# Performance work log

Measured on AMD Instinct MI355X. Metric: run time of the kernel, lower is better.

## Reference

```python
import jax, jax.numpy as jnp
import numpy as np

B, H = 1, 512
NVAR, NCLS = 16384, 65536
NP, NM = 4096, 4096
NEG = -1e30


def setup_inputs() -> dict:
    key = jax.random.key(0)
    ks = jax.random.split(key, 16)
    s = 0.02  # weight init scale
    return {
        "literal_emb": jax.random.normal(ks[0], (B, 2 * NVAR, H), jnp.float32),
        "clause_emb": jax.random.normal(ks[1], (B, NCLS, H), jnp.float32),
        "pos_idx": jax.random.randint(ks[2], (NP,), 0, NCLS),
        "neg_idx": jax.random.randint(ks[3], (NM,), 0, NCLS),
        "keep_mask": jax.random.randint(ks[4], (NP, NM), 0, 2).astype(bool),
        "taken_mask": jax.random.uniform(ks[5], (NP, NM)) < 0.01,  # sparse exclusion set
        "var_K_w": s * jax.random.normal(ks[6], (H, H), jnp.float32),
        "var_K_b": jnp.zeros((H,), jnp.float32),
        "var_Q_w": s * jax.random.normal(ks[7], (H, H), jnp.float32),
        "var_Q_b": jnp.zeros((H,), jnp.float32),
        "var_attn_w": s * jax.random.normal(ks[8], (1, H), jnp.float32),
        "var_attn_b": jnp.zeros((1,), jnp.float32),
        "W_Q_w": s * jax.random.normal(ks[9], (H, H), jnp.float32),
        "W_Q_b": jnp.zeros((H,), jnp.float32),
        "W_K_w": s * jax.random.normal(ks[10], (H, H), jnp.float32),
        "W_K_b": jnp.zeros((H,), jnp.float32),
    }


def reference(literal_emb, clause_emb, pos_idx, neg_idx, keep_mask, taken_mask,
              var_K_w, var_K_b, var_Q_w, var_Q_b, var_attn_w, var_attn_b,
              W_Q_w, W_Q_b, W_K_w, W_K_b):
    n_vars = literal_emb.shape[1] // 2
    # --- select_var: additive attention over positive literals ---
    K = literal_emb[:, :n_vars]                       # [B, V, H]
    K_t = K @ var_K_w.T + var_K_b                     # [B, V, H]
    Q = clause_emb.sum(axis=1)                        # [B, H] (C_aggr='sum')
    Q_t = Q @ var_Q_w.T + var_Q_b                     # [B, H]
    u = (jnp.tanh(K_t + Q_t[:, None, :]) @ var_attn_w.T + var_attn_b)[..., 0]  # [B, V]
    log_score = jax.nn.log_softmax(u, axis=-1)
    var_logp = jnp.max(log_score, axis=-1)            # [B]
    var_idx = jnp.argmax(log_score, axis=-1)          # [B]
    # --- clause-pair attention over pivot pos/neg clause pools ---
    q = clause_emb[:, pos_idx] @ W_Q_w.T + W_Q_b      # [B, NP, H]
    k = clause_emb[:, neg_idx] @ W_K_w.T + W_K_b      # [B, NM, H]
    h = q.shape[-1]
    scores = jnp.einsum('bnh,bmh->bnm', q, k) / jnp.sqrt(jnp.float32(h))
    # mask_grid_asym: drop invalid (keep_mask==0) and already-taken pairs, log-normalize
    valid = keep_mask & (~taken_mask)                 # [NP, NM]
    masked = jnp.where(valid[None], scores, jnp.float32(NEG))
    flat = masked.reshape(masked.shape[0], -1)        # [B, NP*NM]
    logp = jax.nn.log_softmax(flat, axis=-1)
    C_logp = jnp.max(logp, axis=-1)                   # [B]
    C_flat = jnp.argmax(logp, axis=-1)                # [B]
    M = scores.shape[-1]
    ci, cj = C_flat // M, C_flat % M
    c_idx_pos = pos_idx[ci]                           # map back to global clause ids
    c_idx_neg = neg_idx[cj]
    c_logp = C_logp + var_logp                        # [B]
    return (c_logp, c_idx_pos, c_idx_neg, var_idx)
```

## Files before the change

### kernel.cpp

```cpp
#include <hip/hip_runtime.h>
#include <hip/hip_bf16.h>
#include <math.h>

#define HH 512
#define NVARS 16384
#define NPOS 4096
#define NMS 4096
#define NEGV -1.0e30f
#define RSQRT_H 0.04419417382415922f

typedef unsigned short u16;
typedef __attribute__((ext_vector_type(8))) short bf16x8;
typedef __attribute__((ext_vector_type(4))) float f32x4;

struct SPart { float m; float s; int a; int pad; };

__device__ inline u16 f2bf(float f) {
  unsigned u = __float_as_uint(f);
  unsigned r = (u + 0x7fffu + ((u >> 16) & 1u)) >> 16;
  return (u16)r;
}
__device__ inline float bf2f(u16 h) { return __uint_as_float(((unsigned)h) << 16); }

__device__ inline void wreduce_maxidx(float& v, int& idx) {
#pragma unroll
  for (int m = 1; m < 64; m <<= 1) {
    float ov = __shfl_xor(v, m, 64);
    int oi = __shfl_xor(idx, m, 64);
    if (ov > v || (ov == v && oi < idx)) { v = ov; idx = oi; }
  }
}

__device__ inline float wreduce_sum(float v) {
#pragma unroll
  for (int m = 1; m < 64; m <<= 1) v += __shfl_xor(v, m, 64);
  return v;
}

__device__ __forceinline__ void stage_frag(const u16* src, u16* dst) {
  __builtin_amdgcn_global_load_lds(
      (const __attribute__((address_space(1))) void*)src,
      (__attribute__((address_space(3))) void*)dst, 16, 0, 0);
}

__device__ __forceinline__ void do_tofrag(
    const float* __restrict__ src, u16* __restrict__ hi, u16* __restrict__ lo,
    int frag, int lane) {
  const int R = frag >> 4, K = frag & 15;
  const float* p = src + (size_t)(R * 16 + (lane & 15)) * HH + K * 32 + (lane >> 4) * 8;
  float v[8];
  *(float4*)&v[0] = *(const float4*)p;
  *(float4*)&v[4] = *(const float4*)(p + 4);
  u16 h[8], l[8];
#pragma unroll
  for (int e = 0; e < 8; ++e) { h[e] = f2bf(v[e]); l[e] = f2bf(v[e] - bf2f(h[e])); }
  size_t base = (size_t)frag * 512 + (size_t)lane * 8;
  *(ushort4*)(hi + base) = *(ushort4*)&h[0];
  *(ushort4*)(hi + base + 4) = *(ushort4*)&h[4];
  *(ushort4*)(lo + base) = *(ushort4*)&l[0];
  *(ushort4*)(lo + base + 4) = *(ushort4*)&l[4];
}

__global__ __launch_bounds__(256) void prep_kernel(
    const void* __restrict__ keep, const void* __restrict__ taken,
    unsigned long long* __restrict__ vmask,
    const float* __restrict__ clause, double* __restrict__ qpart,
    const float* __restrict__ lit, u16* __restrict__ lithi, u16* __restrict__ litlo,
    const float* __restrict__ varKw, u16* __restrict__ wkhi, u16* __restrict__ wklo,
    const float* __restrict__ WQw, u16* __restrict__ pwqhi, u16* __restrict__ pwqlo,
    const float* __restrict__ WKw, u16* __restrict__ pwkhi, u16* __restrict__ pwklo) {
  const int bid = blockIdx.x;
  const int t = threadIdx.x;
  if (bid < 1024) {
    const int fg = t & 127;
    const int rh = t >> 7;
    const float* base = clause + (size_t)(bid * 64 + rh * 32) * HH + fg * 4;
    double a0 = 0.0, a1 = 0.0, a2 = 0.0, a3 = 0.0;
    for (int r0 = 0; r0 < 32; r0 += 8) {
      float4 v[8];
#pragma unroll
      for (int u = 0; u < 8; ++u)
        v[u] = *(const float4*)(base + (size_t)(r0 + u) * HH);
#pragma unroll
      for (int u = 0; u < 8; ++u) {
        a0 += (double)v[u].x; a1 += (double)v[u].y;
        a2 += (double)v[u].z; a3 += (double)v[u].w;
      }
    }
    double* o = qpart + (size_t)(bid * 2 + rh) * HH + fg * 4;
    o[0] = a0; o[1] = a1; o[2] = a2; o[3] = a3;
  } else if (bid < 5120) {
    const int frag = (bid - 1024) * 4 + (t >> 6);
    do_tofrag(lit, lithi, litlo, frag, t & 63);
  } else if (bid < 9216) {
    __shared__ unsigned short us[256];
    const int row = bid - 5120;
    const unsigned* kw = (const unsigned*)keep;
    int f = 1;
#pragma unroll
    for (int i = 0; i < 16; ++i) f &= (kw[i] <= 1u);
    const size_t e = (size_t)row * 4096 + (size_t)t * 16;
    unsigned b = 0;
    if (f) {
      const unsigned* kp = (const unsigned*)keep + e;
      const unsigned* tp = (const unsigned*)taken + e;
#pragma unroll
      for (int c = 0; c < 4; ++c) {
        uint4 kv = *(const uint4*)(kp + c * 4);
        uint4 tv = *(const uint4*)(tp + c * 4);
        b |= (unsigned)(kv.x && !tv.x) << (c * 4 + 0);
        b |= (unsigned)(kv.y && !tv.y) << (c * 4 + 1);
        b |= (unsigned)(kv.z && !tv.z) << (c * 4 + 2);
        b |= (unsigned)(kv.w && !tv.w) << (c * 4 + 3);
      }
    } else {
      uint4 kv = *(const uint4*)((const unsigned char*)keep + e);
      uint4 tv = *(const uint4*)((const unsigned char*)taken + e);
      unsigned kws[4] = {kv.x, kv.y, kv.z, kv.w};
      unsigned tws[4] = {tv.x, tv.y, tv.z, tv.w};
#pragma unroll
      for (int c = 0; c < 4; ++c)
#pragma unroll
        for (int y = 0; y < 4; ++y) {
          unsigned kb = (kws[c] >> (8 * y)) & 0xffu;
          unsigned tb = (tws[c] >> (8 * y)) & 0xffu;
          b |= (unsigned)(kb && !tb) << (c * 4 + y);
        }
    }
    us[t] = (unsigned short)b;
    __syncthreads();
    if (t < 64) {
      unsigned long long m =
          (unsigned long long)us[t * 4 + 0] |
          ((unsigned long long)us[t * 4 + 1] << 16) |
          ((unsigned long long)us[t * 4 + 2] << 32) |
          ((unsigned long long)us[t * 4 + 3] << 48);
      vmask[(size_t)row * 64 + t] = m;
    }
  } else {
    const int wb = bid - 9216;
    const int m = wb >> 7;
    const int frag = (wb & 127) * 4 + (t >> 6);
    const float* src = (m == 0) ? varKw : (m == 1) ? WQw : WKw;
    u16* hi = (m == 0) ? wkhi : (m == 1) ? pwqhi : pwkhi;
    u16* lo = (m == 0) ? wklo : (m == 1) ? pwqlo : pwklo;
    do_tofrag(src, hi, lo, frag, t & 63);
  }
}

__global__ __launch_bounds__(256) void qred_kernel(
    const double* __restrict__ qpart, double* __restrict__ Qd) {
  __shared__ double red[256];
  const int t = threadIdx.x;
  const int h = blockIdx.x * 16 + (t & 15);
  const int chunk = t >> 4;
  double s = 0.0;
  for (int j0 = 0; j0 < 128; j0 += 8) {
    double v[8];
#pragma unroll
    for (int u = 0; u < 8; ++u)
      v[u] = qpart[(size_t)(chunk * 128 + j0 + u) * HH + h];
#pragma unroll
    for (int u = 0; u < 8; ++u) s += v[u];
  }
  red[t] = s;
  __syncthreads();
  for (int off = 8; off > 0; off >>= 1) {
    if (chunk < off) red[t] += red[t + off * 16];
    __syncthreads();
  }
  if (t < 16) Qd[blockIdx.x * 16 + t] = red[t];
}

__global__ __launch_bounds__(256) void prepmv_kernel(
    const double* __restrict__ Qd, const float* __restrict__ varQw,
    const float* __restrict__ varQb, const float* __restrict__ varKb,
    float* __restrict__ tvec) {
  __shared__ double red[256];
  const int t = threadIdx.x;
  const int h = blockIdx.x * 16 + (t & 15);
  const int chunk = t >> 4;
  const float* wrow = varQw + (size_t)h * HH + chunk * 32;
  const double* qd = Qd + chunk * 32;
  double s = 0.0;
  for (int j = 0; j < 32; ++j) s += qd[j] * (double)wrow[j];
  red[t] = s;
  __syncthreads();
  for (int off = 8; off > 0; off >>= 1) {
    if (chunk < off) red[t] += red[t + off * 16];
    __syncthreads();
  }
  if (t < 16) {
    int hh = blockIdx.x * 16 + t;
    tvec[hh] = (float)(red[t] + (double)varQb[hh] + (double)varKb[hh]);
  }
}

#define MFMA16(A, B)                                                                 \
  _Pragma("unroll") for (int i_ = 0; i_ < 4; ++i_)                                   \
  _Pragma("unroll") for (int j_ = 0; j_ < 4; ++j_)                                   \
    acc[i_][j_] = __builtin_amdgcn_mfma_f32_16x16x32_bf16(A[i_], B[j_], acc[i_][j_], 0, 0, 0);

#define MFMAS(AH, AL, BH, BL)                                                        \
  do { MFMA16(AH, BH) MFMA16(AH, BL) MFMA16(AL, BH) } while (0)

__global__ __launch_bounds__(256, 3) void proj_kernel(
    const float* __restrict__ clause,
    const int* __restrict__ pos_idx, const int* __restrict__ neg_idx,
    const u16* __restrict__ pwqhi, const u16* __restrict__ pwqlo,
    const u16* __restrict__ pwkhi, const u16* __restrict__ pwklo,
    const float* __restrict__ bQ, const float* __restrict__ bK,
    u16* __restrict__ qhi, u16* __restrict__ qlo,
    u16* __restrict__ khi, u16* __restrict__ klo) {
  const int* __restrict__ idx = blockIdx.z ? neg_idx : pos_idx;
  const u16* __restrict__ whp = blockIdx.z ? pwkhi : pwqhi;
  const u16* __restrict__ wlp = blockIdx.z ? pwklo : pwqlo;
  const float* __restrict__ bias = blockIdx.z ? bK : bQ;
  u16* __restrict__ ohi = blockIdx.z ? khi : qhi;
  u16* __restrict__ olo = blockIdx.z ? klo : qlo;

  const int t = threadIdx.x, lane = t & 63, wid = t >> 6;
  const int wn = wid & 1, wm = wid >> 1;
  const int row0 = blockIdx.x * 128;
  const int col0 = blockIdx.y * 128;

  const float* bptr[4];
#pragma unroll
  for (int j = 0; j < 4; ++j) {
    int g = idx[row0 + wn * 64 + j * 16 + (lane & 15)];
    bptr[j] = clause + (size_t)g * HH + (lane >> 4) * 8;
  }
  const size_t abase = (size_t)((col0 >> 4) + wm * 4) * 8192 + (size_t)lane * 8;

  f32x4 acc[4][4] = {};
#pragma unroll
  for (int s = 0; s < 16; ++s) {
    float rB[4][8];
    bf16x8 aH[4], aL[4], bH[4], bL[4];
#pragma unroll
    for (int f = 0; f < 4; ++f) {
      *(float4*)&rB[f][0] = *(const float4*)(bptr[f] + s * 32);
      *(float4*)&rB[f][4] = *(const float4*)(bptr[f] + s * 32 + 4);
      size_t oa = abase + (size_t)f * 8192 + (size_t)s * 512;
      aH[f] = *(const bf16x8*)(whp + oa);
      aL[f] = *(const bf16x8*)(wlp + oa);
    }
#pragma unroll
    for (int f = 0; f < 4; ++f)
#pragma unroll
      for (int e = 0; e < 8; ++e) {
        float v = rB[f][e];
        u16 h = f2bf(v);
        bH[f][e] = (short)h;
        bL[f][e] = (short)f2bf(v - bf2f(h));
      }
    MFMA16(aH, bH)
    MFMA16(aL, bH)
    MFMA16(aH, bL)
  }

  const int q4 = lane >> 4;
#pragma unroll
  for (int i = 0; i < 4; ++i) {
    const int hbase = col0 + wm * 64 + i * 16 + q4 * 4;
    float b0 = bias[hbase + 0], b1 = bias[hbase + 1];
    float b2 = bias[hbase + 2], b3 = bias[hbase + 3];
    const int lane16 = (lane & 15) + ((i & 1) * 2 + (q4 >> 1)) * 16;
    const int sub = (q4 & 1) * 4;
#pragma unroll
    for (int j = 0; j < 4; ++j) {
      const int frag = ((row0 + wn * 64 + j * 16) >> 4) * 16 +
                       ((col0 + wm * 64 + i * 16) >> 5);
      size_t base = (size_t)frag * 512 + (size_t)lane16 * 8 + sub;
      ushort4 hv, lv;
      float v;
      v = acc[i][j][0] + b0; hv.x = f2bf(v); lv.x = f2bf(v - bf2f(hv.x));
      v = acc[i][j][1] + b1; hv.y = f2bf(v); lv.y = f2bf(v - bf2f(hv.y));
      v = acc[i][j][2] + b2; hv.z = f2bf(v); lv.z = f2bf(v - bf2f(hv.z));
      v = acc[i][j][3] + b3; hv.w = f2bf(v); lv.w = f2bf(v - bf2f(hv.w));
      *(ushort4*)(ohi + base) = hv;
      *(ushort4*)(olo + base) = lv;
    }
  }
}

__global__ __launch_bounds__(256, 2) void ktu_kernel(
    const u16* __restrict__ lithi, const u16* __restrict__ litlo,
    const u16* __restrict__ wkhi, const u16* __restrict__ wklo,
    const float* __restrict__ tvec, const float* __restrict__ attnw,
    float* __restrict__ upart) {
  __shared__ __align__(16) u16 lds[2][4][8][512];
  const int t = threadIdx.x, lane = t & 63, wid = t >> 6;
  const int wn = wid & 1, wm = wid >> 1;
  const int row0 = blockIdx.x * 128;
  const int l8 = lane * 8;

  const u16* sa = (wid == 0) ? lithi : (wid == 1) ? litlo : (wid == 2) ? wkhi : wklo;
  const int rb = (wid < 2) ? (row0 >> 4) : (blockIdx.y * 8);
  const u16* sab = sa + (size_t)rb * 8192 + l8;

#define KSTAGE(buf, s)                                                        \
  _Pragma("unroll") for (int f_ = 0; f_ < 8; ++f_)                            \
    stage_frag(sab + (size_t)f_ * 8192 + (size_t)(s) * 512,                   \
               &lds[buf][wid][f_][0]);

  KSTAGE(0, 0)
  f32x4 acc[4][4] = {};
#pragma unroll
  for (int s = 0; s < 16; ++s) {
    __syncthreads();
    if (s < 15) { KSTAGE((s + 1) & 1, s + 1) }
    const int b = s & 1;
    bf16x8 aH[4], aL[4], bH[4], bL[4];
#pragma unroll
    for (int f = 0; f < 4; ++f) {
      aH[f] = *(const bf16x8*)&lds[b][0][wn * 4 + f][l8];
      aL[f] = *(const bf16x8*)&lds[b][1][wn * 4 + f][l8];
      bH[f] = *(const bf16x8*)&lds[b][2][wm * 4 + f][l8];
      bL[f] = *(const bf16x8*)&lds[b][3][wm * 4 + f][l8];
    }
    MFMAS(aH, aL, bH, bL);
  }
#undef KSTAGE

  const int cbase = blockIdx.y * 128 + wm * 64;
  float tv[4], aw[4];
#pragma unroll
  for (int j = 0; j < 4; ++j) {
    int c = cbase + j * 16 + (lane & 15);
    tv[j] = tvec[c]; aw[j] = attnw[c];
  }
  float us[4][4];
#pragma unroll
  for (int i = 0; i < 4; ++i)
#pragma unroll
    for (int r = 0; r < 4; ++r) {
      float s = 0.f;
#pragma unroll
      for (int j = 0; j < 4; ++j) {
        float x = acc[i][j][r] + tv[j];
        float th = 1.0f - 2.0f / (__expf(2.0f * x) + 1.0f);
        s += th * aw[j];
      }
      us[i][r] = s;
    }
#pragma unroll
  for (int m = 1; m < 16; m <<= 1)
#pragma unroll
    for (int i = 0; i < 4; ++i)
#pragma unroll
      for (int r = 0; r < 4; ++r) us[i][r] += __shfl_xor(us[i][r], m, 64);
  if ((lane & 15) == 0) {
#pragma unroll
    for (int i = 0; i < 4; ++i)
#pragma unroll
      for (int r = 0; r < 4; ++r) {
        int row = row0 + wn * 64 + i * 16 + (lane >> 4) * 4 + r;
        upart[(size_t)(blockIdx.y * 2 + wm) * NVARS + row] = us[i][r];
      }
  }
}

__global__ __launch_bounds__(256, 2) void scores_kernel(
    const u16* __restrict__ qhi, const u16* __restrict__ qlo,
    const u16* __restrict__ khi, const u16* __restrict__ klo,
    const unsigned long long* __restrict__ vmask, SPart* __restrict__ parts) {
  __shared__ __align__(16) u16 lds[2][4][8][512];
  __shared__ unsigned long long mrow[128][2];
  __shared__ float s_rv[4]; __shared__ int s_ri[4]; __shared__ float s_rs[4];
  __shared__ float s_bm; __shared__ int s_ba;

  const int t = threadIdx.x;
  const int lane = t & 63;
  const int wid = t >> 6;
  const int wn = wid & 1, wm = wid >> 1;
  const int l8 = lane * 8;

  const int bid = blockIdx.x;
  const int xcd = bid & 7, p = bid >> 3;
  const int sp = p >> 6, q = p & 63;
  const int g = xcd * 2 + sp;
  const int bx = (g & 3) * 8 + (q & 7);
  const int by = (g >> 2) * 8 + (q >> 3);

  const int n0 = by * 128;
  const int m0 = bx * 128;

  const u16* sa = (wid == 0) ? qhi : (wid == 1) ? qlo : (wid == 2) ? khi : klo;
  const int rb = (wid < 2) ? (n0 >> 4) : (m0 >> 4);
  const u16* sab = sa + (size_t)rb * 8192 + l8;

#define SSTAGE(buf, s)                                                        \
  _Pragma("unroll") for (int f_ = 0; f_ < 8; ++f_)                            \
    stage_frag(sab + (size_t)f_ * 8192 + (size_t)(s) * 512,                   \
               &lds[buf][wid][f_][0]);

  {
    int r = t >> 1, w = t & 1;
    mrow[r][w] = vmask[(size_t)(n0 + r) * (NMS / 64) + (m0 >> 6) + w];
  }

  SSTAGE(0, 0)
  f32x4 acc[4][4] = {};
#pragma unroll
  for (int s = 0; s < 16; ++s) {
    __syncthreads();
    if (s < 15) { SSTAGE((s + 1) & 1, s + 1) }
    const int b = s & 1;
    bf16x8 aH[4], aL[4], bH[4], bL[4];
#pragma unroll
    for (int f = 0; f < 4; ++f) {
      aH[f] = *(const bf16x8*)&lds[b][0][wn * 4 + f][l8];
      aL[f] = *(const bf16x8*)&lds[b][1][wn * 4 + f][l8];
      bH[f] = *(const bf16x8*)&lds[b][2][wm * 4 + f][l8];
      bL[f] = *(const bf16x8*)&lds[b][3][wm * 4 + f][l8];
    }
    MFMAS(aH, aL, bH, bL);
  }
#undef SSTAGE

  const int rbase = wn * 64 + (lane >> 4) * 4;
  const int cb15 = (lane & 15);

  float mv = NEGV; int mi = 0x7fffffff;
#pragma unroll
  for (int i = 0; i < 4; ++i) {
#pragma unroll
    for (int r = 0; r < 4; ++r) {
      int rl = rbase + i * 16 + r;
      unsigned long long ww = mrow[rl][wm];
      int gb = (n0 + rl) * NMS + m0;
#pragma unroll
      for (int j = 0; j < 4; ++j) {
        int bit = j * 16 + cb15;
        int cl = wm * 64 + bit;
        float sv = acc[i][j][r] * RSQRT_H;
        acc[i][j][r] = sv;
        bool valid = ((ww >> bit) & 1ull) != 0;
        if (valid && (sv > mv || (sv == mv && gb + cl < mi))) { mv = sv; mi = gb + cl; }
      }
    }
  }
  wreduce_maxidx(mv, mi);
  if ((t & 63) == 0) { s_rv[wid] = mv; s_ri[wid] = mi; }
  __syncthreads();
  if (t == 0) {
    float bm = s_rv[0]; int ba = s_ri[0];
    for (int w = 1; w < 4; ++w)
      if (s_rv[w] > bm || (s_rv[w] == bm && s_ri[w] < ba)) { bm = s_rv[w]; ba = s_ri[w]; }
    s_bm = bm; s_ba = ba;
  }
  __syncthreads();
  const float bm = s_bm;

  float se = 0.f;
#pragma unroll
  for (int i = 0; i < 4; ++i) {
#pragma unroll
    for (int r = 0; r < 4; ++r) {
      int rl = rbase + i * 16 + r;
      unsigned long long ww = mrow[rl][wm];
#pragma unroll
      for (int j = 0; j < 4; ++j) {
        int bit = j * 16 + cb15;
        bool valid = ((ww >> bit) & 1ull) != 0;
        if (valid) se += __expf(acc[i][j][r] - bm);
      }
    }
  }
  se = wreduce_sum(se);
  if ((t & 63) == 0) s_rs[wid] = se;
  __syncthreads();
  if (t == 0) {
    SPart pt;
    pt.m = s_bm;
    pt.s = s_rs[0] + s_rs[1] + s_rs[2] + s_rs[3];
    pt.a = s_ba; pt.pad = 0;
    parts[by * 32 + bx] = pt;
  }
}

__global__ __launch_bounds__(256) void usum_kernel(
    const float* __restrict__ upart, SPart* __restrict__ uparts2) {
  __shared__ float s_rv[4]; __shared__ int s_ri[4]; __shared__ float s_rs[4];
  __shared__ float s_bm; __shared__ int s_ba;
  const int t = threadIdx.x;
  const int i = blockIdx.x * 256 + t;
  float u = 0.f;
#pragma unroll
  for (int p = 0; p < 8; ++p) u += upart[(size_t)p * NVARS + i];
  float mv = u; int mi = i;
  wreduce_maxidx(mv, mi);
  if ((t & 63) == 0) { s_rv[t >> 6] = mv; s_ri[t >> 6] = mi; }
  __syncthreads();
  if (t == 0) {
    float bm = s_rv[0]; int ba = s_ri[0];
    for (int w = 1; w < 4; ++w)
      if (s_rv[w] > bm || (s_rv[w] == bm && s_ri[w] < ba)) { bm = s_rv[w]; ba = s_ri[w]; }
    s_bm = bm; s_ba = ba;
  }
  __syncthreads();
  float se = __expf(u - s_bm);
  se = wreduce_sum(se);
  if ((t & 63) == 0) s_rs[t >> 6] = se;
  __syncthreads();
  if (t == 0) {
    SPart p;
    p.m = s_bm;
    p.s = s_rs[0] + s_rs[1] + s_rs[2] + s_rs[3];
    p.a = s_ba; p.pad = 0;
    uparts2[blockIdx.x] = p;
  }
}

__global__ __launch_bounds__(256) void final_kernel(
    const SPart* __restrict__ uparts2, const SPart* __restrict__ parts,
    const int* __restrict__ pos_idx, const int* __restrict__ neg_idx,
    float* __restrict__ out) {
  __shared__ float s_rv[4]; __shared__ int s_ri[4]; __shared__ float s_rs[4];
  __shared__ float s_umax; __shared__ int s_uarg; __shared__ float s_usum;
  __shared__ float s_gm; __shared__ int s_ga;
  const int t = threadIdx.x;

  float mv = -3.0e38f; int mi = 0x7fffffff;
  SPart up;
  if (t < 64) {
    up = uparts2[t];
    mv = up.m; mi = up.a;
  }
  wreduce_maxidx(mv, mi);
  if ((t & 63) == 0) { s_rv[t >> 6] = mv; s_ri[t >> 6] = mi; }
  __syncthreads();
  if (t == 0) {
    float bm = s_rv[0]; int ba = s_ri[0];
    for (int w = 1; w < 4; ++w)
      if (s_rv[w] > bm || (s_rv[w] == bm && s_ri[w] < ba)) { bm = s_rv[w]; ba = s_ri[w]; }
    s_umax = bm; s_uarg = ba;
  }
  __syncthreads();
  float se = (t < 64) ? up.s * __expf(up.m - s_umax) : 0.f;
  se = wreduce_sum(se);
  if ((t & 63) == 0) s_rs[t >> 6] = se;
  __syncthreads();
  if (t == 0) s_usum = s_rs[0] + s_rs[1] + s_rs[2] + s_rs[3];
  __syncthreads();

  mv = NEGV; mi = 0x7fffffff;
  for (int i = t; i < 1024; i += 256) {
    SPart p = parts[i];
    if (p.m > mv || (p.m == mv && p.a < mi)) { mv = p.m; mi = p.a; }
  }
  wreduce_maxidx(mv, mi);
  if ((t & 63) == 0) { s_rv[t >> 6] = mv; s_ri[t >> 6] = mi; }
  __syncthreads();
  if (t == 0) {
    float bm = s_rv[0]; int ba = s_ri[0];
    for (int w = 1; w < 4; ++w)
      if (s_rv[w] > bm || (s_rv[w] == bm && s_ri[w] < ba)) { bm = s_rv[w]; ba = s_ri[w]; }
    s_gm = bm; s_ga = ba;
  }
  __syncthreads();
  const float gm = s_gm;
  float ss = 0.f;
  for (int i = t; i < 1024; i += 256) {
    SPart p = parts[i];
    ss += p.s * __expf(p.m - gm);
  }
  ss = wreduce_sum(ss);
  if ((t & 63) == 0) s_rs[t >> 6] = ss;
  __syncthreads();
  if (t == 0) {
    float gsum = s_rs[0] + s_rs[1] + s_rs[2] + s_rs[3];
    float c_logp = -logf(gsum) - logf(s_usum);
    int ga = s_ga;
    if (ga == 0x7fffffff) ga = 0;
    int ci = ga >> 12, cj = ga & 4095;
    out[0] = c_logp;
    out[1] = (float)pos_idx[ci];
    out[2] = (float)neg_idx[cj];
    out[3] = (float)s_uarg;
  }
}

extern "C" void kernel_launch(void* const* d_in, const int* in_sizes, int n_in,
                              void* d_out, int out_size, void* d_ws, size_t ws_size,
                              hipStream_t stream) {
  (void)in_sizes; (void)n_in; (void)out_size; (void)ws_size;
  const float* lit    = (const float*)d_in[0];
  const float* clause = (const float*)d_in[1];
  const int* pos_idx  = (const int*)d_in[2];
  const int* neg_idx  = (const int*)d_in[3];
  const void* keep    = d_in[4];
  const void* taken   = d_in[5];
  const float* varKw  = (const float*)d_in[6];
  const float* varKb  = (const float*)d_in[7];
  const float* varQw  = (const float*)d_in[8];
  const float* varQb  = (const float*)d_in[9];
  const float* attnw  = (const float*)d_in[10];
  const float* WQw    = (const float*)d_in[12];
  const float* WQb    = (const float*)d_in[13];
  const float* WKw    = (const float*)d_in[14];
  const float* WKb    = (const float*)d_in[15];

  char* ws = (char*)d_ws;
  size_t off = 0;
  auto alloc = [&](size_t b) {
    char* p = ws + off;
    off = (off + b + 255) & ~(size_t)255;
    return p;
  };
  double* qpart              = (double*)alloc((size_t)2048 * HH * 8);
  double* Qd                 = (double*)alloc(HH * 8);
  float* tvec                = (float*)alloc(HH * 4);
  float* upart               = (float*)alloc(8 * (size_t)NVARS * 4);
  unsigned long long* vmask  = (unsigned long long*)alloc((size_t)NPOS * (NMS / 64) * 8);
  u16* qhi                   = (u16*)alloc((size_t)NPOS * HH * 2);
  u16* qlo                   = (u16*)alloc((size_t)NPOS * HH * 2);
  u16* khi                   = (u16*)alloc((size_t)NMS * HH * 2);
  u16* klo                   = (u16*)alloc((size_t)NMS * HH * 2);
  u16* wkhi                  = (u16*)alloc((size_t)HH * HH * 2);
  u16* wklo                  = (u16*)alloc((size_t)HH * HH * 2);
  u16* pwqhi                 = (u16*)alloc((size_t)HH * HH * 2);
  u16* pwqlo                 = (u16*)alloc((size_t)HH * HH * 2);
  u16* pwkhi                 = (u16*)alloc((size_t)HH * HH * 2);
  u16* pwklo                 = (u16*)alloc((size_t)HH * HH * 2);
  u16* lithi                 = (u16*)alloc((size_t)NVARS * HH * 2);
  u16* litlo                 = (u16*)alloc((size_t)NVARS * HH * 2);
  SPart* parts               = (SPart*)alloc(1024 * sizeof(SPart));
  SPart* uparts2             = (SPart*)alloc(64 * sizeof(SPart));

  prep_kernel<<<9600, 256, 0, stream>>>(keep, taken, vmask, clause, qpart,
                                        lit, lithi, litlo,
                                        varKw, wkhi, wklo,
                                        WQw, pwqhi, pwqlo,
                                        WKw, pwkhi, pwklo);
  qred_kernel<<<32, 256, 0, stream>>>(qpart, Qd);
  prepmv_kernel<<<32, 256, 0, stream>>>(Qd, varQw, varQb, varKb, tvec);
  proj_kernel<<<dim3(32, 4, 2), 256, 0, stream>>>(clause, pos_idx, neg_idx,
                                                  pwqhi, pwqlo, pwkhi, pwklo,
                                                  WQb, WKb,
                                                  qhi, qlo, khi, klo);
  ktu_kernel<<<dim3(128, 4), 256, 0, stream>>>(lithi, litlo, wkhi, wklo,
                                               tvec, attnw, upart);
  scores_kernel<<<1024, 256, 0, stream>>>(qhi, qlo, khi, klo, vmask, parts);
  usum_kernel<<<64, 256, 0, stream>>>(upart, uparts2);
  final_kernel<<<1, 256, 0, stream>>>(uparts2, parts, pos_idx, neg_idx,
                                      (float*)d_out);
}
```

Before: 218.9 us.

## Split prep kernel, reorder launches, and enlarge per-thread streaming work

```diff
diff --git a/kernel.cpp b/kernel.cpp
--- a/kernel.cpp
+++ b/kernel.cpp
@@ -61,65 +61,78 @@
   *(ushort4*)(lo + base + 4) = *(ushort4*)&l[4];
 }
 
-__global__ __launch_bounds__(256) void prep_kernel(
-    const void* __restrict__ keep, const void* __restrict__ taken,
-    unsigned long long* __restrict__ vmask,
-    const float* __restrict__ clause, double* __restrict__ qpart,
-    const float* __restrict__ lit, u16* __restrict__ lithi, u16* __restrict__ litlo,
+__global__ __launch_bounds__(256) void wtofrag_kernel(
     const float* __restrict__ varKw, u16* __restrict__ wkhi, u16* __restrict__ wklo,
     const float* __restrict__ WQw, u16* __restrict__ pwqhi, u16* __restrict__ pwqlo,
     const float* __restrict__ WKw, u16* __restrict__ pwkhi, u16* __restrict__ pwklo) {
+  const int wb = blockIdx.x;
+  const int m = wb >> 7;
+  const int frag = (wb & 127) * 4 + (threadIdx.x >> 6);
+  const float* src = (m == 0) ? varKw : (m == 1) ? WQw : WKw;
+  u16* hi = (m == 0) ? wkhi : (m == 1) ? pwqhi : pwkhi;
+  u16* lo = (m == 0) ? wklo : (m == 1) ? pwqlo : pwklo;
+  do_tofrag(src, hi, lo, frag, threadIdx.x & 63);
+}
+
+__global__ __launch_bounds__(256) void stream_kernel(
+    const float* __restrict__ clause, double* __restrict__ qpart,
+    const float* __restrict__ lit, u16* __restrict__ lithi, u16* __restrict__ litlo,
+    const void* __restrict__ keep, const void* __restrict__ taken,
+    unsigned long long* __restrict__ vmask) {
   const int bid = blockIdx.x;
   const int t = threadIdx.x;
-  if (bid < 1024) {
+  if (bid < 2048) {
     const int fg = t & 127;
     const int rh = t >> 7;
-    const float* base = clause + (size_t)(bid * 64 + rh * 32) * HH + fg * 4;
+    const float* base = clause + ((size_t)bid * 32 + rh * 16) * HH + fg * 4;
+    float4 v[16];
+#pragma unroll
+    for (int u = 0; u < 16; ++u)
+      v[u] = *(const float4*)(base + (size_t)u * HH);
     double a0 = 0.0, a1 = 0.0, a2 = 0.0, a3 = 0.0;
-    for (int r0 = 0; r0 < 32; r0 += 8) {
-      float4 v[8];
-#pragma unroll
-      for (int u = 0; u < 8; ++u)
-        v[u] = *(const float4*)(base + (size_t)(r0 + u) * HH);
-#pragma unroll
-      for (int u = 0; u < 8; ++u) {
-        a0 += (double)v[u].x; a1 += (double)v[u].y;
-        a2 += (double)v[u].z; a3 += (double)v[u].w;
-      }
+#pragma unroll
+    for (int u = 0; u < 16; ++u) {
+      a0 += (double)v[u].x; a1 += (double)v[u].y;
+      a2 += (double)v[u].z; a3 += (double)v[u].w;
     }
     double* o = qpart + (size_t)(bid * 2 + rh) * HH + fg * 4;
     o[0] = a0; o[1] = a1; o[2] = a2; o[3] = a3;
-  } else if (bid < 5120) {
-    const int frag = (bid - 1024) * 4 + (t >> 6);
+  } else if (bid < 6144) {
+    const int frag = (bid - 2048) * 4 + (t >> 6);
     do_tofrag(lit, lithi, litlo, frag, t & 63);
-  } else if (bid < 9216) {
-    __shared__ unsigned short us[256];
-    const int row = bid - 5120;
+  } else {
+    __shared__ unsigned half_[256];
+    const int pb = bid - 6144;
     const unsigned* kw = (const unsigned*)keep;
     int f = 1;
 #pragma unroll
     for (int i = 0; i < 16; ++i) f &= (kw[i] <= 1u);
-    const size_t e = (size_t)row * 4096 + (size_t)t * 16;
+    const size_t e = (size_t)pb * 8192 + (size_t)t * 32;
     unsigned b = 0;
     if (f) {
       const unsigned* kp = (const unsigned*)keep + e;
       const unsigned* tp = (const unsigned*)taken + e;
-#pragma unroll
-      for (int c = 0; c < 4; ++c) {
-        uint4 kv = *(const uint4*)(kp + c * 4);
-        uint4 tv = *(const uint4*)(tp + c * 4);
-        b |= (unsigned)(kv.x && !tv.x) << (c * 4 + 0);
-        b |= (unsigned)(kv.y && !tv.y) << (c * 4 + 1);
-        b |= (unsigned)(kv.z && !tv.z) << (c * 4 + 2);
-        b |= (unsigned)(kv.w && !tv.w) << (c * 4 + 3);
+      uint4 kv[8], tv[8];
+#pragma unroll
+      for (int c = 0; c < 8; ++c) { kv[c] = *(const uint4*)(kp + c * 4); }
+#pragma unroll
+      for (int c = 0; c < 8; ++c) { tv[c] = *(const uint4*)(tp + c * 4); }
+#pragma unroll
+      for (int c = 0; c < 8; ++c) {
+        b |= (unsigned)(kv[c].x && !tv[c].x) << (c * 4 + 0);
+        b |= (unsigned)(kv[c].y && !tv[c].y) << (c * 4 + 1);
+        b |= (unsigned)(kv[c].z && !tv[c].z) << (c * 4 + 2);
+        b |= (unsigned)(kv[c].w && !tv[c].w) << (c * 4 + 3);
       }
     } else {
-      uint4 kv = *(const uint4*)((const unsigned char*)keep + e);
-      uint4 tv = *(const uint4*)((const unsigned char*)taken + e);
-      unsigned kws[4] = {kv.x, kv.y, kv.z, kv.w};
-      unsigned tws[4] = {tv.x, tv.y, tv.z, tv.w};
-#pragma unroll
-      for (int c = 0; c < 4; ++c)
+      const unsigned char* kp = (const unsigned char*)keep + e;
+      const unsigned char* tp = (const unsigned char*)taken + e;
+      uint4 k0 = *(const uint4*)kp, k1 = *(const uint4*)(kp + 16);
+      uint4 t0 = *(const uint4*)tp, t1 = *(const uint4*)(tp + 16);
+      unsigned kws[8] = {k0.x, k0.y, k0.z, k0.w, k1.x, k1.y, k1.z, k1.w};
+      unsigned tws[8] = {t0.x, t0.y, t0.z, t0.w, t1.x, t1.y, t1.z, t1.w};
+#pragma unroll
+      for (int c = 0; c < 8; ++c)
 #pragma unroll
         for (int y = 0; y < 4; ++y) {
           unsigned kb = (kws[c] >> (8 * y)) & 0xffu;
@@ -127,24 +140,13 @@
           b |= (unsigned)(kb && !tb) << (c * 4 + y);
         }
     }
-    us[t] = (unsigned short)b;
+    half_[t] = b;
     __syncthreads();
-    if (t < 64) {
-      unsigned long long m =
-          (unsigned long long)us[t * 4 + 0] |
-          ((unsigned long long)us[t * 4 + 1] << 16) |
-          ((unsigned long long)us[t * 4 + 2] << 32) |
-          ((unsigned long long)us[t * 4 + 3] << 48);
-      vmask[(size_t)row * 64 + t] = m;
-    }
-  } else {
-    const int wb = bid - 9216;
-    const int m = wb >> 7;
-    const int frag = (wb & 127) * 4 + (t >> 6);
-    const float* src = (m == 0) ? varKw : (m == 1) ? WQw : WKw;
-    u16* hi = (m == 0) ? wkhi : (m == 1) ? pwqhi : pwkhi;
-    u16* lo = (m == 0) ? wklo : (m == 1) ? pwqlo : pwklo;
-    do_tofrag(src, hi, lo, frag, t & 63);
+    if (t < 128) {
+      unsigned long long m = (unsigned long long)half_[t * 2] |
+                             ((unsigned long long)half_[t * 2 + 1] << 32);
+      vmask[(size_t)pb * 128 + t] = m;
+    }
   }
 }
 
@@ -155,11 +157,11 @@
   const int h = blockIdx.x * 16 + (t & 15);
   const int chunk = t >> 4;
   double s = 0.0;
-  for (int j0 = 0; j0 < 128; j0 += 8) {
+  for (int j0 = 0; j0 < 256; j0 += 8) {
     double v[8];
 #pragma unroll
     for (int u = 0; u < 8; ++u)
-      v[u] = qpart[(size_t)(chunk * 128 + j0 + u) * HH + h];
+      v[u] = qpart[(size_t)(chunk * 256 + j0 + u) * HH + h];
 #pragma unroll
     for (int u = 0; u < 8; ++u) s += v[u];
   }
@@ -609,7 +611,7 @@
     off = (off + b + 255) & ~(size_t)255;
     return p;
   };
-  double* qpart              = (double*)alloc((size_t)2048 * HH * 8);
+  double* qpart              = (double*)alloc((size_t)4096 * HH * 8);
   double* Qd                 = (double*)alloc(HH * 8);
   float* tvec                = (float*)alloc(HH * 4);
   float* upart               = (float*)alloc(8 * (size_t)NVARS * 4);
@@ -629,20 +631,20 @@
   SPart* parts               = (SPart*)alloc(1024 * sizeof(SPart));
   SPart* uparts2             = (SPart*)alloc(64 * sizeof(SPart));
 
-  prep_kernel<<<9600, 256, 0, stream>>>(keep, taken, vmask, clause, qpart,
-                                        lit, lithi, litlo,
-                                        varKw, wkhi, wklo,
-                                        WQw, pwqhi, pwqlo,
-                                        WKw, pwkhi, pwklo);
-  qred_kernel<<<32, 256, 0, stream>>>(qpart, Qd);
-  prepmv_kernel<<<32, 256, 0, stream>>>(Qd, varQw, varQb, varKb, tvec);
+  wtofrag_kernel<<<384, 256, 0, stream>>>(varKw, wkhi, wklo,
+                                          WQw, pwqhi, pwqlo,
+                                          WKw, pwkhi, pwklo);
   proj_kernel<<<dim3(32, 4, 2), 256, 0, stream>>>(clause, pos_idx, neg_idx,
                                                   pwqhi, pwqlo, pwkhi, pwklo,
                                                   WQb, WKb,
                                                   qhi, qlo, khi, klo);
+  stream_kernel<<<8192, 256, 0, stream>>>(clause, qpart, lit, lithi, litlo,
+                                          keep, taken, vmask);
+  qred_kernel<<<32, 256, 0, stream>>>(qpart, Qd);
+  prepmv_kernel<<<32, 256, 0, stream>>>(Qd, varQw, varQb, varKb, tvec);
+  scores_kernel<<<1024, 256, 0, stream>>>(qhi, qlo, khi, klo, vmask, parts);
   ktu_kernel<<<dim3(128, 4), 256, 0, stream>>>(lithi, litlo, wkhi, wklo,
                                                tvec, attnw, upart);
-  scores_kernel<<<1024, 256, 0, stream>>>(qhi, qlo, khi, klo, vmask, parts);
   usum_kernel<<<64, 256, 0, stream>>>(upart, uparts2);
   final_kernel<<<1, 256, 0, stream>>>(uparts2, parts, pos_idx, neg_idx,
                                       (float*)d_out);
```

New measurement: 246.1 us. +12.4%, slower.
